# Optimization experiments

Measured on AMD Instinct MI355X. Metric: run time of the kernel, lower is better.

Reference implementation:

```python
import jax, jax.numpy as jnp
import numpy as np

EMB_DIM = 1024
ATTN_DIM = 1024


def setup_inputs() -> dict:
    key = jax.random.key(0)
    k_x, k_wk, k_wq, k_wv = jax.random.split(key, 4)
    bound = 1.0 / np.sqrt(EMB_DIM)  # nn.Linear default init range
    return {
        "embedded": jax.random.normal(k_x, (4, 2048, EMB_DIM), dtype=jnp.float32),
        "W_k": jax.random.uniform(k_wk, (ATTN_DIM, EMB_DIM), jnp.float32, -bound, bound),
        "W_q": jax.random.uniform(k_wq, (ATTN_DIM, EMB_DIM), jnp.float32, -bound, bound),
        "W_v": jax.random.uniform(k_wv, (ATTN_DIM, EMB_DIM), jnp.float32, -bound, bound),
    }


def reference(embedded, W_k, W_q, W_v):
    # Linear (bias=False): y = x @ W.T
    K = jnp.einsum("bse,ae->bsa", embedded, W_k)
    Q = jnp.einsum("bse,ae->bsa", embedded, W_q)
    V = jnp.einsum("bse,ae->bsa", embedded, W_v)
    S = K.shape[1]
    scale = 1.0 / jnp.sqrt(jnp.float32(ATTN_DIM))
    scores = jnp.einsum("bqa,bka->bqk", Q, K) * scale  # [B, S, S]
    causal = jnp.tril(jnp.ones((S, S), dtype=bool))  # True = keep
    scores = jnp.where(causal[None, :, :], scores, -jnp.inf)
    attn = jax.nn.softmax(scores, axis=2)
    out = jnp.einsum("bqk,bka->bqa", attn, V)
    # torch.round(x, decimals=4)
    return jnp.round(out * 1e4) / 1e4
```

## Files before the change

### kernel.cpp

```cpp
#include <hip/hip_runtime.h>
#include <stdint.h>

#define B_ 4
#define S_ 2048
#define E_ 1024
#define D_ 1024

typedef short  bf16x8 __attribute__((ext_vector_type(8)));
typedef float  f32x4  __attribute__((ext_vector_type(4)));

static __device__ __forceinline__ unsigned short f2bf(float f) {
    unsigned int u = __float_as_uint(f);
    u += 0x7fffu + ((u >> 16) & 1u);
    return (unsigned short)(u >> 16);
}

static __device__ __forceinline__ void async16(const unsigned short* g, unsigned short* l) {
    auto gp = (const __attribute__((address_space(1))) void*)(uintptr_t)g;
    auto lp = (__attribute__((address_space(3))) void*)(uintptr_t)l;
    __builtin_amdgcn_global_load_lds(gp, lp, 16, 0, 0);
}


__global__ __launch_bounds__(256)
void convert_kernel(const float* __restrict__ x,  const float* __restrict__ Wk,
                    const float* __restrict__ Wq, const float* __restrict__ Wv,
                    unsigned short* __restrict__ xb, unsigned short* __restrict__ Wb)
{
    const long long idx = ((long long)blockIdx.x * 256 + threadIdx.x) * 4;
    const float* src; unsigned short* dst; long long off;
    if (idx < (long long)B_ * S_ * E_) {
        src = x; dst = xb; off = idx;
    } else {
        long long w = idx - (long long)B_ * S_ * E_;
        const int sel = (int)(w >> 20);
        off = w & 1048575LL;
        src = (sel == 0) ? Wk : (sel == 1) ? Wq : Wv;
        dst = Wb + ((long long)sel << 20);
    }
    const float4 f = *(const float4*)(src + off);
    ushort4 u = { f2bf(f.x), f2bf(f.y), f2bf(f.z), f2bf(f.w) };
    *(ushort4*)(dst + off) = u;
}

__global__ __launch_bounds__(256, 4)
void proj_kernel(const unsigned short* __restrict__ xb,
                 const unsigned short* __restrict__ Wb,
                 unsigned short* __restrict__ Qb,
                 unsigned short* __restrict__ Kb,
                 unsigned short* __restrict__ Vt)
{
    __shared__ __align__(16) unsigned short As[128 * 64];
    __shared__ __align__(16) unsigned short Bs[128 * 64];

    const int t    = threadIdx.x;
    const int m0   = blockIdx.x * 128;
    const int ny   = blockIdx.y;
    const int wsel = ny >> 3;
    const int nloc = (ny & 7) * 128;

    const int lane = t & 63, wave = t >> 6;
    const int l15 = lane & 15, quad = lane >> 4;
    const int wm = wave & 1, wn = wave >> 1;
    const int sr = lane >> 3;
    const int sq = ((lane & 7) ^ sr) * 8;
    const int l7 = l15 & 7;
    const int rcA0 = (wm * 64 + l15) * 64 + ((quad ^ l7) * 8);
    const int rcA1 = (wm * 64 + l15) * 64 + (((4 + quad) ^ l7) * 8);
    const int rcB0 = (wn * 64 + l15) * 64 + ((quad ^ l7) * 8);
    const int rcB1 = (wn * 64 + l15) * 64 + (((4 + quad) ^ l7) * 8);

    const unsigned short* gA = xb + (size_t)(m0 + wave * 32 + sr) * E_ + sq;
    const unsigned short* gB = Wb + (size_t)(ny * 128 + wave * 32 + sr) * E_ + sq;
    unsigned short* lA = &As[wave * 2048];
    unsigned short* lB = &Bs[wave * 2048];

    f32x4 acc[4][4];
    #pragma unroll
    for (int i = 0; i < 4; i++)
        #pragma unroll
        for (int j = 0; j < 4; j++) acc[i][j] = {0.f, 0.f, 0.f, 0.f};

    for (int k0 = 0; k0 < E_; k0 += 64) {
        __syncthreads();
        #pragma unroll
        for (int i = 0; i < 4; i++) {
            async16(gA + k0 + i * 8 * E_, lA + i * 512);
            async16(gB + k0 + i * 8 * E_, lB + i * 512);
        }
        __syncthreads();

        #pragma unroll
        for (int s = 0; s < 2; s++) {
            bf16x8 af[4], bfr[4];
            const int ra = s ? rcA1 : rcA0, rb = s ? rcB1 : rcB0;
            #pragma unroll
            for (int i = 0; i < 4; i++) af[i]  = *(const bf16x8*)&As[ra + i * 1024];
            #pragma unroll
            for (int j = 0; j < 4; j++) bfr[j] = *(const bf16x8*)&Bs[rb + j * 1024];
            #pragma unroll
            for (int i = 0; i < 4; i++)
                #pragma unroll
                for (int j = 0; j < 4; j++)
                    acc[i][j] = __builtin_amdgcn_mfma_f32_16x16x32_bf16(af[i], bfr[j], acc[i][j], 0, 0, 0);
        }
    }

    if (wsel == 0) {
        #pragma unroll
        for (int i = 0; i < 4; i++)
            #pragma unroll
            for (int j = 0; j < 4; j++) {
                const int gn = nloc + wn * 64 + j * 16 + l15;
                #pragma unroll
                for (int r = 0; r < 4; r++) {
                    const int gm = m0 + wm * 64 + i * 16 + quad * 4 + r;
                    Kb[(size_t)gm * D_ + gn] = f2bf(acc[i][j][r]);
                }
            }
    } else if (wsel == 1) {
        #pragma unroll
        for (int i = 0; i < 4; i++)
            #pragma unroll
            for (int j = 0; j < 4; j++) {
                const int gn = nloc + wn * 64 + j * 16 + l15;
                #pragma unroll
                for (int r = 0; r < 4; r++) {
                    const int gm = m0 + wm * 64 + i * 16 + quad * 4 + r;
                    Qb[(size_t)gm * D_ + gn] = f2bf(acc[i][j][r] * 0.03125f);
                }
            }
    } else {
        #pragma unroll
        for (int i = 0; i < 4; i++)
            #pragma unroll
            for (int j = 0; j < 4; j++) {
                const int s0 = m0 + wm * 64 + i * 16 + quad * 4;
                const int b  = s0 >> 11, sl = s0 & (S_ - 1);
                const int gn = nloc + wn * 64 + j * 16 + l15;
                ushort4 u = { f2bf(acc[i][j][0]), f2bf(acc[i][j][1]),
                              f2bf(acc[i][j][2]), f2bf(acc[i][j][3]) };
                *(ushort4*)&Vt[((size_t)(b << 10) + gn) * S_ + sl] = u;
            }
    }
}

__global__ __launch_bounds__(256, 4)
void expscores_kernel(const unsigned short* __restrict__ Qb,
                      const unsigned short* __restrict__ Kb,
                      unsigned short* __restrict__ P,
                      float* __restrict__ rowpart)
{
    const int nt = blockIdx.x;
    const int mt = 15 - blockIdx.y;
    const int b  = blockIdx.z;
    if (nt > mt) return;

    __shared__ __align__(16) unsigned short As[128 * 64];
    __shared__ __align__(16) unsigned short Bs[128 * 64];

    const int t = threadIdx.x;
    const int m0 = mt * 128, n0 = nt * 128;

    const int lane = t & 63, wave = t >> 6;
    const int l15 = lane & 15, quad = lane >> 4;
    const int wm = wave & 1, wn = wave >> 1;
    const int sr = lane >> 3;
    const int sq = ((lane & 7) ^ sr) * 8;
    const int l7 = l15 & 7;

    const unsigned short* gA = Qb + (size_t)b * S_ * D_ + (size_t)(m0 + wave * 32 + sr) * D_ + sq;
    const unsigned short* gB = Kb + (size_t)b * S_ * D_ + (size_t)(n0 + wave * 32 + sr) * D_ + sq;
    unsigned short* lA = &As[wave * 2048];
    unsigned short* lB = &Bs[wave * 2048];

    f32x4 acc[4][4];
    #pragma unroll
    for (int i = 0; i < 4; i++)
        #pragma unroll
        for (int j = 0; j < 4; j++) acc[i][j] = {0.f, 0.f, 0.f, 0.f};

    for (int kt = 0; kt < 16; kt++) {
        const int k0 = kt * 64;
        __syncthreads();
        #pragma unroll
        for (int i = 0; i < 4; i++) {
            async16(gA + k0 + i * 8 * D_, lA + i * 512);
            async16(gB + k0 + i * 8 * D_, lB + i * 512);
        }
        __syncthreads();

        #pragma unroll
        for (int s = 0; s < 2; s++) {
            const int cs = ((s * 4 + quad) ^ l7) * 8;
            bf16x8 af[4], bfr[4];
            #pragma unroll
            for (int i = 0; i < 4; i++)
                af[i] = *(const bf16x8*)&As[(wm * 64 + i * 16 + l15) * 64 + cs];
            #pragma unroll
            for (int j = 0; j < 4; j++)
                bfr[j] = *(const bf16x8*)&Bs[(wn * 64 + j * 16 + l15) * 64 + cs];
            #pragma unroll
            for (int i = 0; i < 4; i++)
                #pragma unroll
                for (int j = 0; j < 4; j++)
                    acc[i][j] = __builtin_amdgcn_mfma_f32_16x16x32_bf16(af[i], bfr[j], acc[i][j], 0, 0, 0);
        }
    }

    unsigned short* Pb = P + (size_t)b * S_ * S_;
    #pragma unroll
    for (int i = 0; i < 4; i++)
        #pragma unroll
        for (int j = 0; j < 4; j++) {
            const int gn = n0 + wn * 64 + j * 16 + l15;
            #pragma unroll
            for (int r = 0; r < 4; r++) {
                const int gm = m0 + wm * 64 + i * 16 + quad * 4 + r;
                const float e = (gn <= gm) ? __expf(acc[i][j][r]) : 0.f;
                acc[i][j][r] = e;
                Pb[(size_t)gm * S_ + gn] = f2bf(e);
            }
        }

    float* rp = rowpart + ((size_t)b * 32 + nt * 2 + wn) * S_;
    #pragma unroll
    for (int i = 0; i < 4; i++) {
        float rsub[4];
        #pragma unroll
        for (int r = 0; r < 4; r++) {
            float s = acc[i][0][r] + acc[i][1][r] + acc[i][2][r] + acc[i][3][r];
            #pragma unroll
            for (int off = 8; off; off >>= 1) s += __shfl_xor(s, off);
            rsub[r] = s;
        }
        if (l15 == 0) {
            #pragma unroll
            for (int r = 0; r < 4; r++)
                rp[m0 + wm * 64 + i * 16 + quad * 4 + r] = rsub[r];
        }
    }
}

__global__ __launch_bounds__(256, 2)
void pv_kernel(const unsigned short* __restrict__ P,
               const unsigned short* __restrict__ Vt,
               const float* __restrict__ rowpart,
               float* __restrict__ out)
{
    const int nt = blockIdx.x;
    const int yy = blockIdx.y;
    const int b  = blockIdx.z;
    const int mt = (b & 2) ? yy : (15 - yy);

    __shared__ __align__(16) unsigned short As[2 * 128 * 64];
    __shared__ __align__(16) unsigned short Bs[2 * 128 * 64];

    const int t = threadIdx.x;
    const int m0 = mt * 128, n0 = nt * 128;
    const int niter = 2 * mt + 2;

    const int lane = t & 63, wave = t >> 6;
    const int l15 = lane & 15, quad = lane >> 4;
    const int wm = wave & 1, wn = wave >> 1;
    const int sr = lane >> 3;
    const int sq = ((lane & 7) ^ sr) * 8;
    const int l7 = l15 & 7;

    const unsigned short* gA = P  + (size_t)b * S_ * S_ + (size_t)(m0 + wave * 32 + sr) * S_ + sq;
    const unsigned short* gB = Vt + (size_t)b * D_ * S_ + (size_t)(n0 + wave * 32 + sr) * S_ + sq;
    unsigned short* lA = &As[wave * 2048];
    unsigned short* lB = &Bs[wave * 2048];

    f32x4 acc[4][4];
    #pragma unroll
    for (int i = 0; i < 4; i++)
        #pragma unroll
        for (int j = 0; j < 4; j++) acc[i][j] = {0.f, 0.f, 0.f, 0.f};

    #pragma unroll
    for (int i = 0; i < 4; i++) {
        async16(gA + i * 8 * S_, lA + i * 512);
        async16(gB + i * 8 * S_, lB + i * 512);
    }

    int buf = 0;
    for (int kt = 0; kt < niter; kt++) {
        __syncthreads();
        if (kt + 1 < niter) {
            const int k0 = (kt + 1) * 64;
            const int nb = (buf ^ 1) * 8192;
            #pragma unroll
            for (int i = 0; i < 4; i++) {
                async16(gA + k0 + i * 8 * S_, lA + nb + i * 512);
                async16(gB + k0 + i * 8 * S_, lB + nb + i * 512);
            }
        }
        const unsigned short* Ac = As + buf * 8192;
        const unsigned short* Bc = Bs + buf * 8192;
        #pragma unroll
        for (int s = 0; s < 2; s++) {
            const int cs = ((s * 4 + quad) ^ l7) * 8;
            bf16x8 af[4], bfr[4];
            #pragma unroll
            for (int i = 0; i < 4; i++)
                af[i] = *(const bf16x8*)&Ac[(wm * 64 + i * 16 + l15) * 64 + cs];
            #pragma unroll
            for (int j = 0; j < 4; j++)
                bfr[j] = *(const bf16x8*)&Bc[(wn * 64 + j * 16 + l15) * 64 + cs];
            #pragma unroll
            for (int i = 0; i < 4; i++)
                #pragma unroll
                for (int j = 0; j < 4; j++)
                    acc[i][j] = __builtin_amdgcn_mfma_f32_16x16x32_bf16(af[i], bfr[j], acc[i][j], 0, 0, 0);
        }
        buf ^= 1;
    }

    const int nsl = 2 * mt + 2;
    const float* rp = rowpart + (size_t)b * 32 * S_ + (m0 + wm * 64 + lane);
    float rsum = 0.f;
    for (int k = 0; k < nsl; k++) rsum += rp[(size_t)k * S_];
    const float invr = 1.0f / rsum;

    #pragma unroll
    for (int i = 0; i < 4; i++) {
        #pragma unroll
        for (int r = 0; r < 4; r++) {
            const float vr = __shfl(invr, i * 16 + quad * 4 + r);
            const int gm = m0 + wm * 64 + i * 16 + quad * 4 + r;
            #pragma unroll
            for (int j = 0; j < 4; j++) {
                const int gn = n0 + wn * 64 + j * 16 + l15;
                out[((size_t)b * S_ + gm) * D_ + gn] = rintf(acc[i][j][r] * vr * 1e4f) * 1e-4f;
            }
        }
    }
}

extern "C" void kernel_launch(void* const* d_in, const int* in_sizes, int n_in,
                              void* d_out, int out_size, void* d_ws, size_t ws_size,
                              hipStream_t stream)
{
    (void)in_sizes; (void)n_in; (void)out_size; (void)ws_size;
    const float* x  = (const float*)d_in[0];
    const float* Wk = (const float*)d_in[1];
    const float* Wq = (const float*)d_in[2];
    const float* Wv = (const float*)d_in[3];
    float* out = (float*)d_out;

    char* ws = (char*)d_ws;
    unsigned short* Qb = (unsigned short*)ws;
    unsigned short* Kb = Qb + (size_t)B_ * S_ * D_;
    unsigned short* Vt = Kb + (size_t)B_ * S_ * D_;
    unsigned short* P  = Vt + (size_t)B_ * D_ * S_;
    unsigned short* xb = P;
    unsigned short* Wb = xb + (size_t)B_ * S_ * E_;
    float* rowpart = (float*)(P + (size_t)B_ * S_ * S_);

    const int conv_blocks = (B_ * S_ * E_ + 3 * D_ * E_) / (256 * 4);
    convert_kernel  <<<conv_blocks, 256, 0, stream>>>(x, Wk, Wq, Wv, xb, Wb);
    proj_kernel     <<<dim3(64, 24, 1),   256, 0, stream>>>(xb, Wb, Qb, Kb, Vt);
    expscores_kernel<<<dim3(16, 16, B_),  256, 0, stream>>>(Qb, Kb, P, rowpart);
    pv_kernel       <<<dim3(8, 16, B_),   256, 0, stream>>>(P, Vt, rowpart, out);
}
```

Baseline: 216.1 us.

## Shrink attention tiles to 128x64 and launch only causal score tiles

```diff
diff --git a/kernel.cpp b/kernel.cpp
--- a/kernel.cpp
+++ b/kernel.cpp
@@ -145,38 +145,34 @@
     }
 }
 
-__global__ __launch_bounds__(256, 4)
+__global__ __launch_bounds__(256, 6)
 void expscores_kernel(const unsigned short* __restrict__ Qb,
                       const unsigned short* __restrict__ Kb,
                       unsigned short* __restrict__ P,
                       float* __restrict__ rowpart)
 {
-    const int nt = blockIdx.x;
-    const int mt = 15 - blockIdx.y;
-    const int b  = blockIdx.z;
-    if (nt > mt) return;
+    int rem = blockIdx.x, mt = 0;
+    while (rem >= 2 * mt + 2) { rem -= 2 * mt + 2; mt++; }
+    const int nt = rem;
+    const int b  = blockIdx.y;
+    const int m0 = mt * 128, n0 = nt * 64;
 
     __shared__ __align__(16) unsigned short As[128 * 64];
-    __shared__ __align__(16) unsigned short Bs[128 * 64];
+    __shared__ __align__(16) unsigned short Bs[64 * 64];
 
     const int t = threadIdx.x;
-    const int m0 = mt * 128, n0 = nt * 128;
-
     const int lane = t & 63, wave = t >> 6;
     const int l15 = lane & 15, quad = lane >> 4;
-    const int wm = wave & 1, wn = wave >> 1;
     const int sr = lane >> 3;
     const int sq = ((lane & 7) ^ sr) * 8;
     const int l7 = l15 & 7;
 
-    const unsigned short* gA = Qb + (size_t)b * S_ * D_ + (size_t)(m0 + wave * 32 + sr) * D_ + sq;
-    const unsigned short* gB = Kb + (size_t)b * S_ * D_ + (size_t)(n0 + wave * 32 + sr) * D_ + sq;
-    unsigned short* lA = &As[wave * 2048];
-    unsigned short* lB = &Bs[wave * 2048];
-
-    f32x4 acc[4][4];
-    #pragma unroll
-    for (int i = 0; i < 4; i++)
+    const unsigned short* gQ = Qb + (size_t)b * S_ * D_ + (size_t)(m0 + sr) * D_ + sq;
+    const unsigned short* gK = Kb + (size_t)b * S_ * D_ + (size_t)(n0 + sr) * D_ + sq;
+
+    f32x4 acc[2][4];
+    #pragma unroll
+    for (int i = 0; i < 2; i++)
         #pragma unroll
         for (int j = 0; j < 4; j++) acc[i][j] = {0.f, 0.f, 0.f, 0.f};
 
@@ -184,24 +180,29 @@
         const int k0 = kt * 64;
         __syncthreads();
         #pragma unroll
-        for (int i = 0; i < 4; i++) {
-            async16(gA + k0 + i * 8 * D_, lA + i * 512);
-            async16(gB + k0 + i * 8 * D_, lB + i * 512);
+        for (int i = 0; i < 6; i++) {
+            if (i < 4) {
+                const int u = wave + i * 4;
+                async16(gQ + (size_t)u * 8 * D_ + k0, &As[u * 512]);
+            } else {
+                const int u = wave + (i - 4) * 4;
+                async16(gK + (size_t)u * 8 * D_ + k0, &Bs[u * 512]);
+            }
         }
         __syncthreads();
 
         #pragma unroll
         for (int s = 0; s < 2; s++) {
             const int cs = ((s * 4 + quad) ^ l7) * 8;
-            bf16x8 af[4], bfr[4];
-            #pragma unroll
-            for (int i = 0; i < 4; i++)
-                af[i] = *(const bf16x8*)&As[(wm * 64 + i * 16 + l15) * 64 + cs];
+            bf16x8 af[2], bfr[4];
+            #pragma unroll
+            for (int i = 0; i < 2; i++)
+                af[i] = *(const bf16x8*)&As[(wave * 32 + i * 16 + l15) * 64 + cs];
             #pragma unroll
             for (int j = 0; j < 4; j++)
-                bfr[j] = *(const bf16x8*)&Bs[(wn * 64 + j * 16 + l15) * 64 + cs];
-            #pragma unroll
-            for (int i = 0; i < 4; i++)
+                bfr[j] = *(const bf16x8*)&Bs[(j * 16 + l15) * 64 + cs];
+            #pragma unroll
+            for (int i = 0; i < 2; i++)
                 #pragma unroll
                 for (int j = 0; j < 4; j++)
                     acc[i][j] = __builtin_amdgcn_mfma_f32_16x16x32_bf16(af[i], bfr[j], acc[i][j], 0, 0, 0);
@@ -210,22 +211,22 @@
 
     unsigned short* Pb = P + (size_t)b * S_ * S_;
     #pragma unroll
-    for (int i = 0; i < 4; i++)
+    for (int i = 0; i < 2; i++)
         #pragma unroll
         for (int j = 0; j < 4; j++) {
-            const int gn = n0 + wn * 64 + j * 16 + l15;
+            const int gn = n0 + j * 16 + l15;
             #pragma unroll
             for (int r = 0; r < 4; r++) {
-                const int gm = m0 + wm * 64 + i * 16 + quad * 4 + r;
+                const int gm = m0 + wave * 32 + i * 16 + quad * 4 + r;
                 const float e = (gn <= gm) ? __expf(acc[i][j][r]) : 0.f;
                 acc[i][j][r] = e;
                 Pb[(size_t)gm * S_ + gn] = f2bf(e);
             }
         }
 
-    float* rp = rowpart + ((size_t)b * 32 + nt * 2 + wn) * S_;
-    #pragma unroll
-    for (int i = 0; i < 4; i++) {
+    float* rp = rowpart + ((size_t)b * 32 + nt) * S_;
+    #pragma unroll
+    for (int i = 0; i < 2; i++) {
         float rsub[4];
         #pragma unroll
         for (int r = 0; r < 4; r++) {
@@ -237,101 +238,90 @@
         if (l15 == 0) {
             #pragma unroll
             for (int r = 0; r < 4; r++)
-                rp[m0 + wm * 64 + i * 16 + quad * 4 + r] = rsub[r];
-        }
-    }
-}
-
-__global__ __launch_bounds__(256, 2)
+                rp[m0 + wave * 32 + i * 16 + quad * 4 + r] = rsub[r];
+        }
+    }
+}
+
+__global__ __launch_bounds__(256, 6)
 void pv_kernel(const unsigned short* __restrict__ P,
                const unsigned short* __restrict__ Vt,
                const float* __restrict__ rowpart,
                float* __restrict__ out)
 {
     const int nt = blockIdx.x;
-    const int yy = blockIdx.y;
+    const int mt = 15 - blockIdx.y;
     const int b  = blockIdx.z;
-    const int mt = (b & 2) ? yy : (15 - yy);
-
-    __shared__ __align__(16) unsigned short As[2 * 128 * 64];
-    __shared__ __align__(16) unsigned short Bs[2 * 128 * 64];
+    const int m0 = mt * 128, n0 = nt * 64;
+    const int niter = 2 * mt + 2;
+
+    __shared__ __align__(16) unsigned short As[128 * 64];
+    __shared__ __align__(16) unsigned short Bs[64 * 64];
 
     const int t = threadIdx.x;
-    const int m0 = mt * 128, n0 = nt * 128;
-    const int niter = 2 * mt + 2;
-
     const int lane = t & 63, wave = t >> 6;
     const int l15 = lane & 15, quad = lane >> 4;
-    const int wm = wave & 1, wn = wave >> 1;
     const int sr = lane >> 3;
     const int sq = ((lane & 7) ^ sr) * 8;
     const int l7 = l15 & 7;
 
-    const unsigned short* gA = P  + (size_t)b * S_ * S_ + (size_t)(m0 + wave * 32 + sr) * S_ + sq;
-    const unsigned short* gB = Vt + (size_t)b * D_ * S_ + (size_t)(n0 + wave * 32 + sr) * S_ + sq;
-    unsigned short* lA = &As[wave * 2048];
-    unsigned short* lB = &Bs[wave * 2048];
-
-    f32x4 acc[4][4];
-    #pragma unroll
-    for (int i = 0; i < 4; i++)
+    const unsigned short* gP = P  + (size_t)b * S_ * S_ + (size_t)(m0 + sr) * S_ + sq;
+    const unsigned short* gV = Vt + (size_t)b * D_ * S_ + (size_t)(n0 + sr) * S_ + sq;
+
+    f32x4 acc[2][4];
+    #pragma unroll
+    for (int i = 0; i < 2; i++)
         #pragma unroll
         for (int j = 0; j < 4; j++) acc[i][j] = {0.f, 0.f, 0.f, 0.f};
 
-    #pragma unroll
-    for (int i = 0; i < 4; i++) {
-        async16(gA + i * 8 * S_, lA + i * 512);
-        async16(gB + i * 8 * S_, lB + i * 512);
-    }
-
-    int buf = 0;
     for (int kt = 0; kt < niter; kt++) {
-        __syncthreads();
-        if (kt + 1 < niter) {
-            const int k0 = (kt + 1) * 64;
-            const int nb = (buf ^ 1) * 8192;
-            #pragma unroll
-            for (int i = 0; i < 4; i++) {
-                async16(gA + k0 + i * 8 * S_, lA + nb + i * 512);
-                async16(gB + k0 + i * 8 * S_, lB + nb + i * 512);
-            }
-        }
-        const unsigned short* Ac = As + buf * 8192;
-        const unsigned short* Bc = Bs + buf * 8192;
+        const int k0 = kt * 64;
+        __syncthreads();
+        #pragma unroll
+        for (int i = 0; i < 6; i++) {
+            if (i < 4) {
+                const int u = wave + i * 4;
+                async16(gP + (size_t)u * 8 * S_ + k0, &As[u * 512]);
+            } else {
+                const int u = wave + (i - 4) * 4;
+                async16(gV + (size_t)u * 8 * S_ + k0, &Bs[u * 512]);
+            }
+        }
+        __syncthreads();
+
         #pragma unroll
         for (int s = 0; s < 2; s++) {
             const int cs = ((s * 4 + quad) ^ l7) * 8;
-            bf16x8 af[4], bfr[4];
-            #pragma unroll
-            for (int i = 0; i < 4; i++)
-                af[i] = *(const bf16x8*)&Ac[(wm * 64 + i * 16 + l15) * 64 + cs];
+            bf16x8 af[2], bfr[4];
+            #pragma unroll
+            for (int i = 0; i < 2; i++)
+                af[i] = *(const bf16x8*)&As[(wave * 32 + i * 16 + l15) * 64 + cs];
             #pragma unroll
             for (int j = 0; j < 4; j++)
-                bfr[j] = *(const bf16x8*)&Bc[(wn * 64 + j * 16 + l15) * 64 + cs];
-            #pragma unroll
-            for (int i = 0; i < 4; i++)
+                bfr[j] = *(const bf16x8*)&Bs[(j * 16 + l15) * 64 + cs];
+            #pragma unroll
+            for (int i = 0; i < 2; i++)
                 #pragma unroll
                 for (int j = 0; j < 4; j++)
                     acc[i][j] = __builtin_amdgcn_mfma_f32_16x16x32_bf16(af[i], bfr[j], acc[i][j], 0, 0, 0);
         }
-        buf ^= 1;
-    }
-
-    const int nsl = 2 * mt + 2;
-    const float* rp = rowpart + (size_t)b * 32 * S_ + (m0 + wm * 64 + lane);
+    }
+
+    const int row32 = lane & 31;
+    const float* rp = rowpart + (size_t)b * 32 * S_ + (m0 + wave * 32 + row32);
     float rsum = 0.f;
-    for (int k = 0; k < nsl; k++) rsum += rp[(size_t)k * S_];
+    for (int k = 0; k < niter; k++) rsum += rp[(size_t)k * S_];
     const float invr = 1.0f / rsum;
 
     #pragma unroll
-    for (int i = 0; i < 4; i++) {
+    for (int i = 0; i < 2; i++) {
         #pragma unroll
         for (int r = 0; r < 4; r++) {
             const float vr = __shfl(invr, i * 16 + quad * 4 + r);
-            const int gm = m0 + wm * 64 + i * 16 + quad * 4 + r;
+            const int gm = m0 + wave * 32 + i * 16 + quad * 4 + r;
             #pragma unroll
             for (int j = 0; j < 4; j++) {
-                const int gn = n0 + wn * 64 + j * 16 + l15;
+                const int gn = n0 + j * 16 + l15;
                 out[((size_t)b * S_ + gm) * D_ + gn] = rintf(acc[i][j][r] * vr * 1e4f) * 1e-4f;
             }
         }
@@ -361,6 +351,6 @@
     const int conv_blocks = (B_ * S_ * E_ + 3 * D_ * E_) / (256 * 4);
     convert_kernel  <<<conv_blocks, 256, 0, stream>>>(x, Wk, Wq, Wv, xb, Wb);
     proj_kernel     <<<dim3(64, 24, 1),   256, 0, stream>>>(xb, Wb, Qb, Kb, Vt);
-    expscores_kernel<<<dim3(16, 16, B_),  256, 0, stream>>>(Qb, Kb, P, rowpart);
-    pv_kernel       <<<dim3(8, 16, B_),   256, 0, stream>>>(P, Vt, rowpart, out);
-}
+    expscores_kernel<<<dim3(272, B_, 1),  256, 0, stream>>>(Qb, Kb, P, rowpart);
+    pv_kernel       <<<dim3(16, 16, B_),  256, 0, stream>>>(P, Vt, rowpart, out);
+}
```

Result: slower. 229.8 us (+6.4%).

## Fuse V projection into causal exp-scores launch to fill idle CUs

Applied to the files above, without the earlier changes.

```diff
diff --git a/kernel.cpp b/kernel.cpp
--- a/kernel.cpp
+++ b/kernel.cpp
@@ -146,6 +146,133 @@
 }
 
 __global__ __launch_bounds__(256, 4)
+void fat_kernel(const unsigned short* __restrict__ Qb,
+                const unsigned short* __restrict__ Kb,
+                const unsigned short* __restrict__ xb,
+                const unsigned short* __restrict__ Wb,
+                unsigned short* __restrict__ P,
+                float* __restrict__ rowpart,
+                unsigned short* __restrict__ Vt)
+{
+    __shared__ __align__(16) unsigned short As[128 * 64];
+    __shared__ __align__(16) unsigned short Bs[128 * 64];
+
+    const int bx = blockIdx.x;
+    const bool is_exp = bx < 544;
+
+    const int t = threadIdx.x;
+    const int lane = t & 63, wave = t >> 6;
+    const int l15 = lane & 15, quad = lane >> 4;
+    const int wm = wave & 1, wn = wave >> 1;
+    const int sr = lane >> 3;
+    const int sq = ((lane & 7) ^ sr) * 8;
+    const int l7 = l15 & 7;
+
+    int b = 0, mt = 0, nt = 0, mb = 0, nb = 0;
+    const unsigned short* gA;
+    const unsigned short* gB;
+    if (is_exp) {
+        b = bx >> 7;
+        b = bx / 136;
+        int rem = bx - b * 136;
+        mt = 0;
+        while (rem >= mt + 1) { rem -= mt + 1; mt++; }
+        nt = rem;
+        gA = Qb + (size_t)b * S_ * D_ + (size_t)(mt * 128 + wave * 32 + sr) * D_ + sq;
+        gB = Kb + (size_t)b * S_ * D_ + (size_t)(nt * 128 + wave * 32 + sr) * D_ + sq;
+    } else {
+        const int idx = bx - 544;
+        mb = idx & 63;
+        nb = idx >> 6;
+        gA = xb + (size_t)(mb * 128 + wave * 32 + sr) * E_ + sq;
+        gB = Wb + ((size_t)2 << 20) + (size_t)(nb * 128 + wave * 32 + sr) * E_ + sq;
+    }
+    unsigned short* lA = &As[wave * 2048];
+    unsigned short* lB = &Bs[wave * 2048];
+
+    f32x4 acc[4][4];
+    #pragma unroll
+    for (int i = 0; i < 4; i++)
+        #pragma unroll
+        for (int j = 0; j < 4; j++) acc[i][j] = {0.f, 0.f, 0.f, 0.f};
+
+    for (int k0 = 0; k0 < 1024; k0 += 64) {
+        __syncthreads();
+        #pragma unroll
+        for (int i = 0; i < 4; i++) {
+            async16(gA + k0 + i * 8 * 1024, lA + i * 512);
+            async16(gB + k0 + i * 8 * 1024, lB + i * 512);
+        }
+        __syncthreads();
+
+        #pragma unroll
+        for (int s = 0; s < 2; s++) {
+            const int cs = ((s * 4 + quad) ^ l7) * 8;
+            bf16x8 af[4], bfr[4];
+            #pragma unroll
+            for (int i = 0; i < 4; i++)
+                af[i] = *(const bf16x8*)&As[(wm * 64 + i * 16 + l15) * 64 + cs];
+            #pragma unroll
+            for (int j = 0; j < 4; j++)
+                bfr[j] = *(const bf16x8*)&Bs[(wn * 64 + j * 16 + l15) * 64 + cs];
+            #pragma unroll
+            for (int i = 0; i < 4; i++)
+                #pragma unroll
+                for (int j = 0; j < 4; j++)
+                    acc[i][j] = __builtin_amdgcn_mfma_f32_16x16x32_bf16(af[i], bfr[j], acc[i][j], 0, 0, 0);
+        }
+    }
+
+    if (is_exp) {
+        const int m0 = mt * 128, n0 = nt * 128;
+        unsigned short* Pb = P + (size_t)b * S_ * S_;
+        #pragma unroll
+        for (int i = 0; i < 4; i++)
+            #pragma unroll
+            for (int j = 0; j < 4; j++) {
+                const int gn = n0 + wn * 64 + j * 16 + l15;
+                #pragma unroll
+                for (int r = 0; r < 4; r++) {
+                    const int gm = m0 + wm * 64 + i * 16 + quad * 4 + r;
+                    const float e = (gn <= gm) ? __expf(acc[i][j][r]) : 0.f;
+                    acc[i][j][r] = e;
+                    Pb[(size_t)gm * S_ + gn] = f2bf(e);
+                }
+            }
+
+        float* rp = rowpart + ((size_t)b * 32 + nt * 2 + wn) * S_;
+        #pragma unroll
+        for (int i = 0; i < 4; i++) {
+            float rsub[4];
+            #pragma unroll
+            for (int r = 0; r < 4; r++) {
+                float s = acc[i][0][r] + acc[i][1][r] + acc[i][2][r] + acc[i][3][r];
+                #pragma unroll
+                for (int off = 8; off; off >>= 1) s += __shfl_xor(s, off);
+                rsub[r] = s;
+            }
+            if (l15 == 0) {
+                #pragma unroll
+                for (int r = 0; r < 4; r++)
+                    rp[m0 + wm * 64 + i * 16 + quad * 4 + r] = rsub[r];
+            }
+        }
+    } else {
+        #pragma unroll
+        for (int i = 0; i < 4; i++)
+            #pragma unroll
+            for (int j = 0; j < 4; j++) {
+                const int s0 = mb * 128 + wm * 64 + i * 16 + quad * 4;
+                const int vb = s0 >> 11, sl = s0 & (S_ - 1);
+                const int gn = nb * 128 + wn * 64 + j * 16 + l15;
+                ushort4 u = { f2bf(acc[i][j][0]), f2bf(acc[i][j][1]),
+                              f2bf(acc[i][j][2]), f2bf(acc[i][j][3]) };
+                *(ushort4*)&Vt[((size_t)(vb << 10) + gn) * S_ + sl] = u;
+            }
+    }
+}
+
+__global__ __launch_bounds__(256, 4)
 void expscores_kernel(const unsigned short* __restrict__ Qb,
                       const unsigned short* __restrict__ Kb,
                       unsigned short* __restrict__ P,
@@ -342,25 +469,45 @@
                               void* d_out, int out_size, void* d_ws, size_t ws_size,
                               hipStream_t stream)
 {
-    (void)in_sizes; (void)n_in; (void)out_size; (void)ws_size;
+    (void)in_sizes; (void)n_in; (void)out_size;
     const float* x  = (const float*)d_in[0];
     const float* Wk = (const float*)d_in[1];
     const float* Wq = (const float*)d_in[2];
     const float* Wv = (const float*)d_in[3];
     float* out = (float*)d_out;
 
+    const size_t SD  = (size_t)B_ * S_ * D_;
+    const size_t SS  = (size_t)B_ * S_ * S_;
+    const size_t XBE = (size_t)B_ * S_ * E_;
+    const size_t WBE = (size_t)3 * D_ * E_;
+    const size_t RP  = (size_t)B_ * 32 * S_;
+
+    const size_t need_fat = (3 * SD + SS + XBE + WBE) * 2 + RP * 4;
+
     char* ws = (char*)d_ws;
     unsigned short* Qb = (unsigned short*)ws;
-    unsigned short* Kb = Qb + (size_t)B_ * S_ * D_;
-    unsigned short* Vt = Kb + (size_t)B_ * S_ * D_;
-    unsigned short* P  = Vt + (size_t)B_ * D_ * S_;
-    unsigned short* xb = P;
-    unsigned short* Wb = xb + (size_t)B_ * S_ * E_;
-    float* rowpart = (float*)(P + (size_t)B_ * S_ * S_);
+    unsigned short* Kb = Qb + SD;
+    unsigned short* Vt = Kb + SD;
+    unsigned short* P  = Vt + SD;
+    unsigned short* xb;
+    unsigned short* Wb;
+    float* rowpart = (float*)(P + SS);
 
     const int conv_blocks = (B_ * S_ * E_ + 3 * D_ * E_) / (256 * 4);
-    convert_kernel  <<<conv_blocks, 256, 0, stream>>>(x, Wk, Wq, Wv, xb, Wb);
-    proj_kernel     <<<dim3(64, 24, 1),   256, 0, stream>>>(xb, Wb, Qb, Kb, Vt);
-    expscores_kernel<<<dim3(16, 16, B_),  256, 0, stream>>>(Qb, Kb, P, rowpart);
-    pv_kernel       <<<dim3(8, 16, B_),   256, 0, stream>>>(P, Vt, rowpart, out);
-}
+
+    if (ws_size >= need_fat) {
+        xb = (unsigned short*)(rowpart + RP);
+        Wb = xb + XBE;
+        convert_kernel  <<<conv_blocks, 256, 0, stream>>>(x, Wk, Wq, Wv, xb, Wb);
+        proj_kernel     <<<dim3(64, 16, 1),  256, 0, stream>>>(xb, Wb, Qb, Kb, Vt);
+        fat_kernel      <<<dim3(1056, 1, 1), 256, 0, stream>>>(Qb, Kb, xb, Wb, P, rowpart, Vt);
+        pv_kernel       <<<dim3(8, 16, B_),  256, 0, stream>>>(P, Vt, rowpart, out);
+    } else {
+        xb = P;
+        Wb = xb + XBE;
+        convert_kernel  <<<conv_blocks, 256, 0, stream>>>(x, Wk, Wq, Wv, xb, Wb);
+        proj_kernel     <<<dim3(64, 24, 1),  256, 0, stream>>>(xb, Wb, Qb, Kb, Vt);
+        expscores_kernel<<<dim3(16, 16, B_), 256, 0, stream>>>(Qb, Kb, P, rowpart);
+        pv_kernel       <<<dim3(8, 16, B_),  256, 0, stream>>>(P, Vt, rowpart, out);
+    }
+}
```

After: 225.5 us. 4.4% more time.
